# Kernel tuning notes

Hardware: AMD Instinct MI355X
Metric: run time of the kernel (lower is better)

## Reference

```python
import jax, jax.numpy as jnp
import numpy as np

N_NODES = 100000
N_EDGES = 1000000
IN_DIM = 128
HID = 128
OUT_DIM = 40


def setup_inputs() -> dict:
    key = jax.random.key(0)
    ks = jax.random.split(key, 16)
    x = jax.random.normal(ks[0], (N_NODES, IN_DIM), dtype=jnp.float32)
    edge_index = jax.random.randint(ks[1], (2, N_EDGES), 0, N_NODES, dtype=jnp.int64)
    s = 0.05
    # GAT layer 1 (in->hid, heads=1, concat=True)
    W1 = jax.random.normal(ks[2], (HID, IN_DIM), jnp.float32) * s
    b1 = jnp.zeros((HID,), jnp.float32)
    att1 = jax.random.normal(ks[3], (1, 2 * HID), jnp.float32) * s
    bias1 = jnp.zeros((HID,), jnp.float32)
    # GAT layer 2 (hid->hid)
    W2 = jax.random.normal(ks[4], (HID, HID), jnp.float32) * s
    b2 = jnp.zeros((HID,), jnp.float32)
    att2 = jax.random.normal(ks[5], (1, 2 * HID), jnp.float32) * s
    bias2 = jnp.zeros((HID,), jnp.float32)
    # post_mp: Linear(hid,hid) -> Dropout -> Linear(hid,out)
    Wp1 = jax.random.normal(ks[6], (HID, HID), jnp.float32) * s
    bp1 = jnp.zeros((HID,), jnp.float32)
    Wp2 = jax.random.normal(ks[7], (OUT_DIM, HID), jnp.float32) * s
    bp2 = jnp.zeros((OUT_DIM,), jnp.float32)
    return dict(x=x, edge_index=edge_index, W1=W1, b1=b1, att1=att1, bias1=bias1,
                W2=W2, b2=b2, att2=att2, bias2=bias2,
                Wp1=Wp1, bp1=bp1, Wp2=Wp2, bp2=bp2)


def gat_layer(x, src, dst, W, b, att, bias, n_nodes):
    # x: [N, Fin] -> h: [N, C] (heads=1, concat=True)
    h = x @ W.T + b
    C = h.shape[1]
    att_i, att_j = att[0, :C], att[0, C:]  # split: first half pairs with x_i (dst), second with x_j (src)
    # per-node scalar projections, then gather per edge (avoids [E,2C] concat)
    e = (h @ att_i)[dst] + (h @ att_j)[src]  # [E]
    e = jnp.where(e > 0, e, 0.2 * e)  # leaky_relu(0.2)
    # segment softmax over destination nodes
    m = jax.ops.segment_max(e, dst, num_segments=n_nodes)
    ex = jnp.exp(e - m[dst])
    denom = jax.ops.segment_sum(ex, dst, num_segments=n_nodes)
    alpha = ex / denom[dst]
    out = jax.ops.segment_sum(h[src] * alpha[:, None], dst, num_segments=n_nodes)
    return out + bias


def reference(x, edge_index, W1, b1, att1, bias1, W2, b2, att2, bias2, Wp1, bp1, Wp2, bp2):
    src, dst = edge_index[0], edge_index[1]
    n = x.shape[0]
    h = jax.nn.relu(gat_layer(x, src, dst, W1, b1, att1, bias1, n))  # dropout p=0 -> identity
    h = jax.nn.relu(gat_layer(h, src, dst, W2, b2, att2, bias2, n))
    y = (h @ Wp1.T + bp1) @ Wp2.T + bp2  # post_mp (eval: dropout identity)
    return jax.nn.log_softmax(y, axis=1)
```

## Files before the change

kernel.cpp:

```cpp
#include <hip/hip_runtime.h>

#define N_NODES 100000
#define N_EDGES 1000000
#define HID 128
#define OUT_DIM 40
#define CSR_W 64
#define CUR_STRIDE 16
#define GEMM_TILES 1563
#define EDGE_BLK 977
#define WC_BLK 21

typedef __attribute__((ext_vector_type(8))) short bf16x8;
typedef __attribute__((ext_vector_type(4))) float f32x4;

__device__ inline unsigned short f2bf(float f) {
    unsigned u = __float_as_uint(f);
    u += 0x7fffu + ((u >> 16) & 1u);
    return (unsigned short)(u >> 16);
}
__device__ inline float bf2f(unsigned short u) {
    return __uint_as_float(((unsigned)u) << 16);
}

__device__ inline float4 ld4(const float* p) { return *(const float4*)p; }
__device__ inline float4 ld4(const unsigned short* p) {
    ushort4 u = *(const ushort4*)p;
    return make_float4(bf2f(u.x), bf2f(u.y), bf2f(u.z), bf2f(u.w));
}

__global__ __launch_bounds__(256) void zero_kernel(float4* __restrict__ p, int n4) {
    int i = blockIdx.x * 256 + threadIdx.x;
    int stride = gridDim.x * 256;
    float4 z = make_float4(0.f, 0.f, 0.f, 0.f);
    for (; i < n4; i += stride) p[i] = z;
}

#define LDA 136
template<typename AT>
__device__ __forceinline__ void gemm_tile_body(
    int tile, const AT* __restrict__ A, const float* __restrict__ W,
    const float* __restrict__ out_bias, const float* __restrict__ in_bias,
    int relu_in, const float* __restrict__ att,
    unsigned short* __restrict__ Cb, float* __restrict__ hi, float* __restrict__ hj,
    int n_rows, unsigned short* As, unsigned short* Ws)
{
    const int t = threadIdx.x;
    const int row0 = tile * 64;

    for (int i = 0; i < 8; i++) {
        int lin = t + i * 256;
        int r = lin >> 5;
        int k = (lin & 31) * 4;
        int gr = row0 + r;
        float4 av = make_float4(0.f, 0.f, 0.f, 0.f);
        if (gr < n_rows) av = ld4(A + (size_t)gr * HID + k);
        if (in_bias) {
            av.x += in_bias[k + 0]; av.y += in_bias[k + 1];
            av.z += in_bias[k + 2]; av.w += in_bias[k + 3];
            if (relu_in) {
                av.x = fmaxf(av.x, 0.f); av.y = fmaxf(av.y, 0.f);
                av.z = fmaxf(av.z, 0.f); av.w = fmaxf(av.w, 0.f);
            }
        }
        ushort4 bv;
        bv.x = f2bf(av.x); bv.y = f2bf(av.y); bv.z = f2bf(av.z); bv.w = f2bf(av.w);
        *(ushort4*)(&As[r * LDA + k]) = bv;
    }
    for (int i = 0; i < 16; i++) {
        int lin = t + i * 256;
        int r = lin >> 5;
        int k = (lin & 31) * 4;
        float4 wv = *(const float4*)(W + (size_t)r * HID + k);
        ushort4 bv;
        bv.x = f2bf(wv.x); bv.y = f2bf(wv.y); bv.z = f2bf(wv.z); bv.w = f2bf(wv.w);
        *(ushort4*)(&Ws[r * LDA + k]) = bv;
    }
    __syncthreads();

    const int wave = t >> 6, lane = t & 63;
    const int lrow = lane & 15, quad = lane >> 4;
    const int wrow = wave * 16;

    f32x4 acc[8];
    #pragma unroll
    for (int ni = 0; ni < 8; ni++) acc[ni] = (f32x4){0.f, 0.f, 0.f, 0.f};

    #pragma unroll
    for (int ks = 0; ks < 4; ks++) {
        const int kb = ks * 32 + quad * 8;
        bf16x8 af = *(bf16x8*)(&As[(wrow + lrow) * LDA + kb]);
        #pragma unroll
        for (int ni = 0; ni < 8; ni++) {
            bf16x8 bfr = *(bf16x8*)(&Ws[(ni * 16 + lrow) * LDA + kb]);
            acc[ni] = __builtin_amdgcn_mfma_f32_16x16x32_bf16(af, bfr, acc[ni], 0, 0, 0);
        }
    }

    float pi[4] = {0.f, 0.f, 0.f, 0.f}, pj[4] = {0.f, 0.f, 0.f, 0.f};
    const int rbase = row0 + wrow + quad * 4;
    #pragma unroll
    for (int ni = 0; ni < 8; ni++) {
        const int col = ni * 16 + lrow;
        const float bo = out_bias[col];
        const float ai = att[col], aj = att[HID + col];
        #pragma unroll
        for (int r = 0; r < 4; r++) {
            float v = acc[ni][r] + bo;
            int gr = rbase + r;
            if (gr < n_rows) Cb[(size_t)gr * HID + col] = f2bf(v);
            pi[r] = fmaf(v, ai, pi[r]);
            pj[r] = fmaf(v, aj, pj[r]);
        }
    }
    #pragma unroll
    for (int o = 1; o < 16; o <<= 1) {
        #pragma unroll
        for (int r = 0; r < 4; r++) {
            pi[r] += __shfl_xor(pi[r], o);
            pj[r] += __shfl_xor(pj[r], o);
        }
    }
    if (lrow == 0) {
        #pragma unroll
        for (int r = 0; r < 4; r++) {
            int gr = rbase + r;
            if (gr < n_rows) { hi[gr] = pi[r]; hj[gr] = pj[r]; }
        }
    }
}

__global__ __launch_bounds__(256) void combined_prep(
    const float* __restrict__ x, const float* __restrict__ W1,
    const float* __restrict__ b1, const float* __restrict__ att1,
    const float* __restrict__ Wp1, const float* __restrict__ bp1,
    const float* __restrict__ Wp2, const float* __restrict__ bp2,
    const int* __restrict__ src, const int* __restrict__ dst,
    unsigned* __restrict__ cursor, int* __restrict__ csr,
    unsigned short* __restrict__ hbuf, float* __restrict__ hi, float* __restrict__ hj,
    float* __restrict__ Wc, float* __restrict__ bc)
{
    __shared__ unsigned short As[64 * LDA];
    __shared__ unsigned short Ws[128 * LDA];
    const int b = blockIdx.x, g = b >> 3, r = b & 7;

    if (r < 3) {
        const int eid = g * 3 + r;
        if (eid >= EDGE_BLK) return;
        int e = eid * 1024 + threadIdx.x;
        #pragma unroll
        for (int j = 0; j < 4; j++, e += 256) {
            if (e < N_EDGES) {
                int d = dst[e], s = src[e];
                unsigned p = atomicAdd(&cursor[d << 4], 1u);
                if (p < CSR_W) __builtin_nontemporal_store(s, &csr[(d << 6) + p]);
            }
        }
        return;
    }
    const int oid = g * 5 + (r - 3);
    if (oid < WC_BLK) {
        int t = oid * 256 + threadIdx.x;
        if (t < OUT_DIM * HID) {
            int o = t >> 7, k = t & 127;
            float s = 0.f;
            for (int j = 0; j < HID; j++) s = fmaf(Wp2[o * HID + j], Wp1[j * HID + k], s);
            Wc[t] = s;
        } else if (t < OUT_DIM * HID + OUT_DIM) {
            int o = t - OUT_DIM * HID;
            float s = bp2[o];
            for (int j = 0; j < HID; j++) s = fmaf(Wp2[o * HID + j], bp1[j], s);
            bc[o] = s;
        }
        return;
    }
    const int tile = oid - WC_BLK;
    if (tile >= GEMM_TILES) return;
    gemm_tile_body<float>(tile, x, W1, b1, nullptr, 0, att1, hbuf, hi, hj, N_NODES, As, Ws);
}

__global__ __launch_bounds__(256) void gemm_mfma_b(
    const unsigned short* __restrict__ A, const float* __restrict__ W,
    const float* __restrict__ out_bias, const float* __restrict__ in_bias,
    const float* __restrict__ att,
    unsigned short* __restrict__ Cb, float* __restrict__ hi, float* __restrict__ hj,
    int n_rows)
{
    __shared__ unsigned short As[64 * LDA];
    __shared__ unsigned short Ws[128 * LDA];
    gemm_tile_body<unsigned short>(blockIdx.x, A, W, out_bias, in_bias, 1, att,
                                   Cb, hi, hj, n_rows, As, Ws);
}

__global__ __launch_bounds__(256) void fused_gat(
    const unsigned* __restrict__ cursor, const int* __restrict__ csr,
    const unsigned short* __restrict__ hb,
    const float* __restrict__ hi, const float* __restrict__ hj,
    unsigned short* __restrict__ out)
{
    const int wave = threadIdx.x >> 6;
    const int lane = threadIdx.x & 63;
    const int d = blockIdx.x * 4 + wave;
    if (d >= N_NODES) return;
    unsigned deg = cursor[d << 4];
    if (deg > CSR_W) deg = CSR_W;
    const int cnt = (int)deg;
    const float hid = hi[d];
    const int base = d << 6;

    int sv = 0;
    float ev = -INFINITY;
    if (lane < cnt) {
        sv = csr[base + lane];
        float e = hid + hj[sv];
        ev = e > 0.f ? e : 0.2f * e;
    }
    float m = ev;
    #pragma unroll
    for (int o = 32; o; o >>= 1) m = fmaxf(m, __shfl_xor(m, o));
    const float exv = (lane < cnt) ? __expf(ev - m) : 0.f;
    float denom = exv;
    #pragma unroll
    for (int o = 32; o; o >>= 1) denom += __shfl_xor(denom, o);

    float accx = 0.f, accy = 0.f;
    const int co = lane * 2;
    int i = 0;
    for (; i + 4 <= cnt; i += 4) {
        const int s0 = __shfl(sv, i),     s1 = __shfl(sv, i + 1);
        const int s2 = __shfl(sv, i + 2), s3 = __shfl(sv, i + 3);
        const float w0 = __shfl(exv, i),     w1 = __shfl(exv, i + 1);
        const float w2 = __shfl(exv, i + 2), w3 = __shfl(exv, i + 3);
        const ushort2 u0 = *(const ushort2*)(hb + (size_t)s0 * HID + co);
        const ushort2 u1 = *(const ushort2*)(hb + (size_t)s1 * HID + co);
        const ushort2 u2 = *(const ushort2*)(hb + (size_t)s2 * HID + co);
        const ushort2 u3 = *(const ushort2*)(hb + (size_t)s3 * HID + co);
        accx = fmaf(w0, bf2f(u0.x), accx); accy = fmaf(w0, bf2f(u0.y), accy);
        accx = fmaf(w1, bf2f(u1.x), accx); accy = fmaf(w1, bf2f(u1.y), accy);
        accx = fmaf(w2, bf2f(u2.x), accx); accy = fmaf(w2, bf2f(u2.y), accy);
        accx = fmaf(w3, bf2f(u3.x), accx); accy = fmaf(w3, bf2f(u3.y), accy);
    }
    for (; i < cnt; i++) {
        const int s = __shfl(sv, i);
        const float w = __shfl(exv, i);
        const ushort2 u = *(const ushort2*)(hb + (size_t)s * HID + co);
        accx = fmaf(w, bf2f(u.x), accx);
        accy = fmaf(w, bf2f(u.y), accy);
    }
    const float inv = cnt ? 1.f / denom : 0.f;
    ushort2 o2;
    o2.x = f2bf(accx * inv);
    o2.y = f2bf(accy * inv);
    *(ushort2*)(out + (size_t)d * HID + co) = o2;
}

#define FS 132
__global__ __launch_bounds__(256) void final_proj(
    const unsigned short* __restrict__ agg, const float* __restrict__ bias2,
    const float* __restrict__ Wc, const float* __restrict__ bc,
    float* __restrict__ out)
{
    __shared__ float As[32 * FS];
    __shared__ float Wcs[OUT_DIM * FS];
    const int t = threadIdx.x;
    const int node0 = blockIdx.x * 32;
    for (int i = 0; i < 5; i++) {
        int lin = t + i * 256;
        int r = lin >> 5;
        int c4 = lin & 31;
        float4 v = *(const float4*)(Wc + r * HID + c4 * 4);
        int lo = r * FS + c4 * 4;
        Wcs[lo + 0] = v.x; Wcs[lo + 1] = v.y; Wcs[lo + 2] = v.z; Wcs[lo + 3] = v.w;
    }
    for (int i = 0; i < 4; i++) {
        int lin = t + i * 256;
        int r = lin >> 5;
        int c4 = lin & 31;
        int node = node0 + r;
        int k = c4 * 4;
        float4 v = make_float4(0.f, 0.f, 0.f, 0.f);
        if (node < N_NODES) v = ld4(agg + (size_t)node * HID + k);
        v.x = fmaxf(v.x + bias2[k + 0], 0.f);
        v.y = fmaxf(v.y + bias2[k + 1], 0.f);
        v.z = fmaxf(v.z + bias2[k + 2], 0.f);
        v.w = fmaxf(v.w + bias2[k + 3], 0.f);
        int lo = r * FS + k;
        As[lo + 0] = v.x; As[lo + 1] = v.y; As[lo + 2] = v.z; As[lo + 3] = v.w;
    }
    __syncthreads();
    const int g = t & 7;
    const int local = t >> 3;
    const int node = node0 + local;
    float acc[5];
    #pragma unroll
    for (int j = 0; j < 5; j++) acc[j] = bc[g * 5 + j];
    for (int k = 0; k < HID; k++) {
        float a = As[local * FS + k];
        #pragma unroll
        for (int j = 0; j < 5; j++)
            acc[j] = fmaf(a, Wcs[(g * 5 + j) * FS + k], acc[j]);
    }
    float mx = acc[0];
    #pragma unroll
    for (int j = 1; j < 5; j++) mx = fmaxf(mx, acc[j]);
    #pragma unroll
    for (int o = 1; o < 8; o <<= 1) mx = fmaxf(mx, __shfl_xor(mx, o));
    float s = 0.f;
    #pragma unroll
    for (int j = 0; j < 5; j++) s += expf(acc[j] - mx);
    #pragma unroll
    for (int o = 1; o < 8; o <<= 1) s += __shfl_xor(s, o);
    float lse = mx + logf(s);
    if (node < N_NODES) {
        #pragma unroll
        for (int j = 0; j < 5; j++)
            out[(size_t)node * OUT_DIM + g * 5 + j] = acc[j] - lse;
    }
}

extern "C" void kernel_launch(void* const* d_in, const int* in_sizes, int n_in,
                              void* d_out, int out_size, void* d_ws, size_t ws_size,
                              hipStream_t stream)
{
    const float* x     = (const float*)d_in[0];
    const int*   ei    = (const int*)d_in[1];
    const float* W1    = (const float*)d_in[2];
    const float* b1    = (const float*)d_in[3];
    const float* att1  = (const float*)d_in[4];
    const float* bias1 = (const float*)d_in[5];
    const float* W2    = (const float*)d_in[6];
    const float* b2    = (const float*)d_in[7];
    const float* att2  = (const float*)d_in[8];
    const float* bias2 = (const float*)d_in[9];
    const float* Wp1   = (const float*)d_in[10];
    const float* bp1   = (const float*)d_in[11];
    const float* Wp2   = (const float*)d_in[12];
    const float* bp2   = (const float*)d_in[13];
    float* out = (float*)d_out;

    const int* src = ei;
    const int* dst = ei + N_EDGES;

    char* ws = (char*)d_ws;
    unsigned short* hbuf = (unsigned short*)ws;
    unsigned short* aggb = hbuf + (size_t)N_NODES * HID;
    float* hi      = (float*)(aggb + (size_t)N_NODES * HID);
    float* hj      = hi + N_NODES;
    unsigned* cursor = (unsigned*)(hj + N_NODES);
    int* csr       = (int*)(cursor + (size_t)N_NODES * CUR_STRIDE);
    float* Wc      = (float*)(csr + (size_t)N_NODES * CSR_W);
    float* bc      = Wc + OUT_DIM * HID;

    const int prep_blocks = 326 * 8;

    zero_kernel<<<512, 256, 0, stream>>>((float4*)cursor, N_NODES * CUR_STRIDE / 4);

    combined_prep<<<prep_blocks, 256, 0, stream>>>(
        x, W1, b1, att1, Wp1, bp1, Wp2, bp2, src, dst,
        cursor, csr, hbuf, hi, hj, Wc, bc);

    fused_gat<<<N_NODES / 4, 256, 0, stream>>>(cursor, csr, hbuf, hi, hj, aggb);

    gemm_mfma_b<<<GEMM_TILES, 256, 0, stream>>>(aggb, W2, b2, bias1, att2, hbuf, hi, hj, N_NODES);
    fused_gat<<<N_NODES / 4, 256, 0, stream>>>(cursor, csr, hbuf, hi, hj, aggb);

    final_proj<<<N_NODES / 32, 256, 0, stream>>>(aggb, bias2, Wc, bc, out);
}
```

Before: 325.4 us.

## Use MFMA for final projection and enlarge layer-2 GEMM tiles to 128 rows

The final projection with log-softmax moves from scalar FP32 FMAs to bf16 MFMA 16x16x32 tiles. The 40 output columns are padded to 48 with zero weights, and the softmax reduction is done across lanes with shuffles. The layer-2 GEMM gets a dedicated kernel that processes 128 rows per block with two M-tiles per wave, halving the number of blocks and the number of times W2 is staged per node. Rounding the final-projection operands to bf16 costs some precision, and the larger tile raises register and LDS use.

After: 313.3 us. 1.04x faster.

```diff
diff --git a/kernel.cpp b/kernel.cpp
--- a/kernel.cpp
+++ b/kernel.cpp
@@ -7,6 +7,8 @@
 #define CSR_W 64
 #define CUR_STRIDE 16
 #define GEMM_TILES 1563
+#define G2_TILES 782
+#define PROJ_TILES 1563
 #define EDGE_BLK 977
 #define WC_BLK 21
 
@@ -178,17 +180,100 @@
     gemm_tile_body<float>(tile, x, W1, b1, nullptr, 0, att1, hbuf, hi, hj, N_NODES, As, Ws);
 }
 
-__global__ __launch_bounds__(256) void gemm_mfma_b(
+__global__ __launch_bounds__(256) void gemm_mfma_b128(
     const unsigned short* __restrict__ A, const float* __restrict__ W,
     const float* __restrict__ out_bias, const float* __restrict__ in_bias,
     const float* __restrict__ att,
     unsigned short* __restrict__ Cb, float* __restrict__ hi, float* __restrict__ hj,
     int n_rows)
 {
-    __shared__ unsigned short As[64 * LDA];
+    __shared__ unsigned short As[128 * LDA];
     __shared__ unsigned short Ws[128 * LDA];
-    gemm_tile_body<unsigned short>(blockIdx.x, A, W, out_bias, in_bias, 1, att,
-                                   Cb, hi, hj, n_rows, As, Ws);
+    const int t = threadIdx.x;
+    const int row0 = blockIdx.x * 128;
+
+    for (int i = 0; i < 16; i++) {
+        int lin = t + i * 256;
+        int r = lin >> 5;
+        int k = (lin & 31) * 4;
+        int gr = row0 + r;
+        float4 av = make_float4(0.f, 0.f, 0.f, 0.f);
+        if (gr < n_rows) av = ld4(A + (size_t)gr * HID + k);
+        av.x = fmaxf(av.x + in_bias[k + 0], 0.f);
+        av.y = fmaxf(av.y + in_bias[k + 1], 0.f);
+        av.z = fmaxf(av.z + in_bias[k + 2], 0.f);
+        av.w = fmaxf(av.w + in_bias[k + 3], 0.f);
+        ushort4 bv;
+        bv.x = f2bf(av.x); bv.y = f2bf(av.y); bv.z = f2bf(av.z); bv.w = f2bf(av.w);
+        *(ushort4*)(&As[r * LDA + k]) = bv;
+    }
+    for (int i = 0; i < 16; i++) {
+        int lin = t + i * 256;
+        int r = lin >> 5;
+        int k = (lin & 31) * 4;
+        float4 wv = *(const float4*)(W + (size_t)r * HID + k);
+        ushort4 bv;
+        bv.x = f2bf(wv.x); bv.y = f2bf(wv.y); bv.z = f2bf(wv.z); bv.w = f2bf(wv.w);
+        *(ushort4*)(&Ws[r * LDA + k]) = bv;
+    }
+    __syncthreads();
+
+    const int wave = t >> 6, lane = t & 63;
+    const int lrow = lane & 15, quad = lane >> 4;
+
+    f32x4 acc[2][8];
+    #pragma unroll
+    for (int mt = 0; mt < 2; mt++)
+        #pragma unroll
+        for (int ni = 0; ni < 8; ni++) acc[mt][ni] = (f32x4){0.f, 0.f, 0.f, 0.f};
+
+    #pragma unroll
+    for (int ks = 0; ks < 4; ks++) {
+        const int kb = ks * 32 + quad * 8;
+        bf16x8 af0 = *(bf16x8*)(&As[(wave * 32 + lrow) * LDA + kb]);
+        bf16x8 af1 = *(bf16x8*)(&As[(wave * 32 + 16 + lrow) * LDA + kb]);
+        #pragma unroll
+        for (int ni = 0; ni < 8; ni++) {
+            bf16x8 bfr = *(bf16x8*)(&Ws[(ni * 16 + lrow) * LDA + kb]);
+            acc[0][ni] = __builtin_amdgcn_mfma_f32_16x16x32_bf16(af0, bfr, acc[0][ni], 0, 0, 0);
+            acc[1][ni] = __builtin_amdgcn_mfma_f32_16x16x32_bf16(af1, bfr, acc[1][ni], 0, 0, 0);
+        }
+    }
+
+    #pragma unroll
+    for (int mt = 0; mt < 2; mt++) {
+        float pi[4] = {0.f, 0.f, 0.f, 0.f}, pj[4] = {0.f, 0.f, 0.f, 0.f};
+        const int rbase = row0 + wave * 32 + mt * 16 + quad * 4;
+        #pragma unroll
+        for (int ni = 0; ni < 8; ni++) {
+            const int col = ni * 16 + lrow;
+            const float bo = out_bias[col];
+            const float ai = att[col], aj = att[HID + col];
+            #pragma unroll
+            for (int r = 0; r < 4; r++) {
+                float v = acc[mt][ni][r] + bo;
+                int gr = rbase + r;
+                if (gr < n_rows) Cb[(size_t)gr * HID + col] = f2bf(v);
+                pi[r] = fmaf(v, ai, pi[r]);
+                pj[r] = fmaf(v, aj, pj[r]);
+            }
+        }
+        #pragma unroll
+        for (int o = 1; o < 16; o <<= 1) {
+            #pragma unroll
+            for (int r = 0; r < 4; r++) {
+                pi[r] += __shfl_xor(pi[r], o);
+                pj[r] += __shfl_xor(pj[r], o);
+            }
+        }
+        if (lrow == 0) {
+            #pragma unroll
+            for (int r = 0; r < 4; r++) {
+                int gr = rbase + r;
+                if (gr < n_rows) { hi[gr] = pi[r]; hj[gr] = pj[r]; }
+            }
+        }
+    }
 }
 
 __global__ __launch_bounds__(256) void fused_gat(
@@ -253,67 +338,99 @@
     *(ushort2*)(out + (size_t)d * HID + co) = o2;
 }
 
-#define FS 132
-__global__ __launch_bounds__(256) void final_proj(
+__global__ __launch_bounds__(256) void final_proj_mfma(
     const unsigned short* __restrict__ agg, const float* __restrict__ bias2,
     const float* __restrict__ Wc, const float* __restrict__ bc,
     float* __restrict__ out)
 {
-    __shared__ float As[32 * FS];
-    __shared__ float Wcs[OUT_DIM * FS];
+    __shared__ unsigned short As[64 * LDA];
+    __shared__ unsigned short Ws[48 * LDA];
     const int t = threadIdx.x;
-    const int node0 = blockIdx.x * 32;
+    const int node0 = blockIdx.x * 64;
+
     for (int i = 0; i < 5; i++) {
         int lin = t + i * 256;
         int r = lin >> 5;
-        int c4 = lin & 31;
-        float4 v = *(const float4*)(Wc + r * HID + c4 * 4);
-        int lo = r * FS + c4 * 4;
-        Wcs[lo + 0] = v.x; Wcs[lo + 1] = v.y; Wcs[lo + 2] = v.z; Wcs[lo + 3] = v.w;
-    }
-    for (int i = 0; i < 4; i++) {
-        int lin = t + i * 256;
-        int r = lin >> 5;
-        int c4 = lin & 31;
-        int node = node0 + r;
-        int k = c4 * 4;
+        int k = (lin & 31) * 4;
+        float4 wv = *(const float4*)(Wc + (size_t)r * HID + k);
+        ushort4 bv;
+        bv.x = f2bf(wv.x); bv.y = f2bf(wv.y); bv.z = f2bf(wv.z); bv.w = f2bf(wv.w);
+        *(ushort4*)(&Ws[r * LDA + k]) = bv;
+    }
+    {
+        int r = 40 + (t >> 5);
+        int k = (t & 31) * 4;
+        ushort4 z; z.x = 0; z.y = 0; z.z = 0; z.w = 0;
+        *(ushort4*)(&Ws[r * LDA + k]) = z;
+    }
+    for (int i = 0; i < 8; i++) {
+        int lin = t + i * 256;
+        int r = lin >> 5;
+        int k = (lin & 31) * 4;
+        int gr = node0 + r;
         float4 v = make_float4(0.f, 0.f, 0.f, 0.f);
-        if (node < N_NODES) v = ld4(agg + (size_t)node * HID + k);
+        if (gr < N_NODES) v = ld4(agg + (size_t)gr * HID + k);
         v.x = fmaxf(v.x + bias2[k + 0], 0.f);
         v.y = fmaxf(v.y + bias2[k + 1], 0.f);
         v.z = fmaxf(v.z + bias2[k + 2], 0.f);
         v.w = fmaxf(v.w + bias2[k + 3], 0.f);
-        int lo = r * FS + k;
-        As[lo + 0] = v.x; As[lo + 1] = v.y; As[lo + 2] = v.z; As[lo + 3] = v.w;
+        ushort4 bv;
+        bv.x = f2bf(v.x); bv.y = f2bf(v.y); bv.z = f2bf(v.z); bv.w = f2bf(v.w);
+        *(ushort4*)(&As[r * LDA + k]) = bv;
     }
     __syncthreads();
-    const int g = t & 7;
-    const int local = t >> 3;
-    const int node = node0 + local;
-    float acc[5];
-    #pragma unroll
-    for (int j = 0; j < 5; j++) acc[j] = bc[g * 5 + j];
-    for (int k = 0; k < HID; k++) {
-        float a = As[local * FS + k];
-        #pragma unroll
-        for (int j = 0; j < 5; j++)
-            acc[j] = fmaf(a, Wcs[(g * 5 + j) * FS + k], acc[j]);
-    }
-    float mx = acc[0];
-    #pragma unroll
-    for (int j = 1; j < 5; j++) mx = fmaxf(mx, acc[j]);
-    #pragma unroll
-    for (int o = 1; o < 8; o <<= 1) mx = fmaxf(mx, __shfl_xor(mx, o));
-    float s = 0.f;
-    #pragma unroll
-    for (int j = 0; j < 5; j++) s += expf(acc[j] - mx);
-    #pragma unroll
-    for (int o = 1; o < 8; o <<= 1) s += __shfl_xor(s, o);
-    float lse = mx + logf(s);
-    if (node < N_NODES) {
-        #pragma unroll
-        for (int j = 0; j < 5; j++)
-            out[(size_t)node * OUT_DIM + g * 5 + j] = acc[j] - lse;
+
+    const int wave = t >> 6, lane = t & 63;
+    const int lrow = lane & 15, quad = lane >> 4;
+    const int wrow = wave * 16;
+
+    f32x4 acc[3];
+    #pragma unroll
+    for (int nt = 0; nt < 3; nt++) acc[nt] = (f32x4){0.f, 0.f, 0.f, 0.f};
+
+    #pragma unroll
+    for (int ks = 0; ks < 4; ks++) {
+        const int kb = ks * 32 + quad * 8;
+        bf16x8 af = *(bf16x8*)(&As[(wrow + lrow) * LDA + kb]);
+        #pragma unroll
+        for (int nt = 0; nt < 3; nt++) {
+            bf16x8 bfr = *(bf16x8*)(&Ws[(nt * 16 + lrow) * LDA + kb]);
+            acc[nt] = __builtin_amdgcn_mfma_f32_16x16x32_bf16(af, bfr, acc[nt], 0, 0, 0);
+        }
+    }
+
+    int cols[3]; float bcv[3]; bool valid[3];
+    #pragma unroll
+    for (int nt = 0; nt < 3; nt++) {
+        cols[nt] = nt * 16 + lrow;
+        valid[nt] = cols[nt] < OUT_DIM;
+        bcv[nt] = valid[nt] ? bc[cols[nt]] : 0.f;
+    }
+    const int rbase = node0 + wrow + quad * 4;
+    #pragma unroll
+    for (int r = 0; r < 4; r++) {
+        float v[3];
+        float mx = -INFINITY;
+        #pragma unroll
+        for (int nt = 0; nt < 3; nt++) {
+            v[nt] = acc[nt][r] + bcv[nt];
+            if (valid[nt]) mx = fmaxf(mx, v[nt]);
+        }
+        #pragma unroll
+        for (int o = 1; o < 16; o <<= 1) mx = fmaxf(mx, __shfl_xor(mx, o));
+        float s = 0.f;
+        #pragma unroll
+        for (int nt = 0; nt < 3; nt++)
+            if (valid[nt]) s += __expf(v[nt] - mx);
+        #pragma unroll
+        for (int o = 1; o < 16; o <<= 1) s += __shfl_xor(s, o);
+        const float lse = mx + __logf(s);
+        const int node = rbase + r;
+        if (node < N_NODES) {
+            #pragma unroll
+            for (int nt = 0; nt < 3; nt++)
+                if (valid[nt]) out[(size_t)node * OUT_DIM + cols[nt]] = v[nt] - lse;
+        }
     }
 }
 
@@ -360,8 +477,8 @@
 
     fused_gat<<<N_NODES / 4, 256, 0, stream>>>(cursor, csr, hbuf, hi, hj, aggb);
 
-    gemm_mfma_b<<<GEMM_TILES, 256, 0, stream>>>(aggb, W2, b2, bias1, att2, hbuf, hi, hj, N_NODES);
+    gemm_mfma_b128<<<G2_TILES, 256, 0, stream>>>(aggb, W2, b2, bias1, att2, hbuf, hi, hj, N_NODES);
     fused_gat<<<N_NODES / 4, 256, 0, stream>>>(cursor, csr, hbuf, hi, hj, aggb);
 
-    final_proj<<<N_NODES / 32, 256, 0, stream>>>(aggb, bias2, Wc, bc, out);
-}
+    final_proj_mfma<<<PROJ_TILES, 256, 0, stream>>>(aggb, bias2, Wc, bc, out);
+}
```
